# Optimization experiments

Hardware: AMD Instinct MI355X
Metric: run time of the kernel (lower is better)

The kernel has to match this reference:

```python
import jax, jax.numpy as jnp
import numpy as np

# Model dims (match init_kwargs): dim=768, num_heads=12, num_kv_heads=2 -> G=6, head_dim=64
DIM, HKV, G, D = 768, 2, 6, 64


def setup_inputs() -> dict:
    key = jax.random.key(0)
    ks = jax.random.split(key, 9)
    w = 0.02  # init scale for weights
    return {
        "x": jax.random.normal(ks[0], (8, 1024, DIM), dtype=jnp.float32),
        "depth_k": jax.random.normal(ks[1], (8, 1024, HKV, D), dtype=jnp.float32),
        "depth_v": jax.random.normal(ks[2], (8, 1024, HKV, D), dtype=jnp.float32),
        "Wq": jax.random.normal(ks[3], (DIM, DIM), dtype=jnp.float32) * w,
        "bq": jnp.zeros((DIM,), dtype=jnp.float32),
        "Wkv": jax.random.normal(ks[4], (2 * HKV * D, DIM), dtype=jnp.float32) * w,
        "bkv": jnp.zeros((2 * HKV * D,), dtype=jnp.float32),
        "Wproj": jax.random.normal(ks[5], (DIM, DIM), dtype=jnp.float32) * w,
        "bproj": jnp.zeros((DIM,), dtype=jnp.float32),
    }


def reference(x, depth_k, depth_v, Wq, bq, Wkv, bkv, Wproj, bproj):
    B, N, C = x.shape
    scale = D ** -0.5
    # Q projection, GQA groups unfolded into the sequence dim: [B, N*G, Hkv, D]
    q = (x @ Wq.T + bq).reshape(B, N * G, HKV, D)
    # KV projection: [B, N, 2, Hkv, D]
    kv = (x @ Wkv.T + bkv).reshape(B, N, 2, HKV, D)
    k, v = kv[:, :, 0], kv[:, :, 1]
    # Concatenate depth (previous-layer) KV cache along the sequence dim
    k_full = jnp.concatenate([depth_k, k], axis=1)  # [B, N_cache+N, Hkv, D]
    v_full = jnp.concatenate([depth_v, v], axis=1)
    # Full (non-causal) attention per kv head over the unfolded query sequence
    scores = jnp.einsum('bqhd,bkhd->bhqk', q, k_full) * scale  # [B, Hkv, N*G, Kv]
    attn = jax.nn.softmax(scores, axis=-1)
    o = jnp.einsum('bhqk,bkhd->bqhd', attn, v_full)  # [B, N*G, Hkv, D]
    out = o.reshape(B, N, C) @ Wproj.T + bproj  # fold G*Hkv*D back to C=dim
    return out, k, v
```

## Files before the change

kernel.cpp:

```cpp
#include <hip/hip_runtime.h>

using sh8 = __attribute__((ext_vector_type(8))) short;
using sh4 = __attribute__((ext_vector_type(4))) short;
using fx4 = __attribute__((ext_vector_type(4))) float;

#define MFMA(a,b,c)   __builtin_amdgcn_mfma_f32_16x16x32_bf16((a),(b),(c),0,0,0)
#define MFMA16(a,b,c) __builtin_amdgcn_mfma_f32_16x16x16bf16_1k((a),(b),(c),0,0,0)

__device__ __forceinline__ short f2bf(float f) {
    union { float f; unsigned u; } v; v.f = f;
    return (short)((v.u + 0x7fffu + ((v.u >> 16) & 1u)) >> 16);
}

__device__ __forceinline__ unsigned bfpair(float lo, float hi) {
    unsigned ul = __float_as_uint(lo) + 0x8000u;
    unsigned uh = __float_as_uint(hi) + 0x8000u;
    return __builtin_amdgcn_perm(uh, ul, 0x07060302);
}

__device__ __forceinline__ sh8 pack8(float4 a, float4 b) {
    union { unsigned u[4]; sh8 s; } r;
    r.u[0] = bfpair(a.x, a.y);
    r.u[1] = bfpair(a.z, a.w);
    r.u[2] = bfpair(b.x, b.y);
    r.u[3] = bfpair(b.z, b.w);
    return r.s;
}

__device__ __forceinline__ sh4 lo4(sh8 v) { return __builtin_shufflevector(v, v, 0, 1, 2, 3); }
__device__ __forceinline__ sh4 hi4(sh8 v) { return __builtin_shufflevector(v, v, 4, 5, 6, 7); }

#define QSCALE 0.18033688011112042f


__global__ __launch_bounds__(256) void qgemm_k(const float* __restrict__ x,
                                               const float* __restrict__ Wq,
                                               const float* __restrict__ bq,
                                               short* __restrict__ q_ws)
{
    __shared__ alignas(16) short Al[128 * 40];
    __shared__ alignas(16) short Bl[128 * 40];
    const int t    = threadIdx.x;
    const int wave = t >> 6, lane = t & 63;
    const int wm   = wave >> 1, wn = wave & 1;
    const int lhi  = lane >> 4, llo = lane & 15;
    const int bm   = blockIdx.y * 128, bn = blockIdx.x * 128;

    const int srow = t >> 1, scol = (t & 1) * 16;
    const float* ap = x  + (size_t)(bm + srow) * 768 + scol;
    const float* bp = Wq + (size_t)(bn + srow) * 768 + scol;

    fx4 zero = {0.f, 0.f, 0.f, 0.f};
    fx4 acc[4][4];
    #pragma unroll
    for (int i = 0; i < 4; ++i)
        #pragma unroll
        for (int j = 0; j < 4; ++j) acc[i][j] = zero;

    float4 pa0 = *(const float4*)(ap);     float4 pa1 = *(const float4*)(ap + 4);
    float4 pa2 = *(const float4*)(ap + 8); float4 pa3 = *(const float4*)(ap + 12);
    float4 pb0 = *(const float4*)(bp);     float4 pb1 = *(const float4*)(bp + 4);
    float4 pb2 = *(const float4*)(bp + 8); float4 pb3 = *(const float4*)(bp + 12);

    for (int k0 = 0; k0 < 768; k0 += 32) {
        __syncthreads();
        *(sh8*)&Al[srow*40 + scol]     = pack8(pa0, pa1);
        *(sh8*)&Al[srow*40 + scol + 8] = pack8(pa2, pa3);
        *(sh8*)&Bl[srow*40 + scol]     = pack8(pb0, pb1);
        *(sh8*)&Bl[srow*40 + scol + 8] = pack8(pb2, pb3);
        __syncthreads();
        if (k0 + 32 < 768) {
            pa0 = *(const float4*)(ap + k0+32);     pa1 = *(const float4*)(ap + k0+36);
            pa2 = *(const float4*)(ap + k0+40);     pa3 = *(const float4*)(ap + k0+44);
            pb0 = *(const float4*)(bp + k0+32);     pb1 = *(const float4*)(bp + k0+36);
            pb2 = *(const float4*)(bp + k0+40);     pb3 = *(const float4*)(bp + k0+44);
        }
        sh8 af[4], bf[4];
        #pragma unroll
        for (int mt = 0; mt < 4; ++mt)
            af[mt] = *(const sh8*)&Al[(wm*64 + mt*16 + llo)*40 + lhi*8];
        #pragma unroll
        for (int nt = 0; nt < 4; ++nt)
            bf[nt] = *(const sh8*)&Bl[(wn*64 + nt*16 + llo)*40 + lhi*8];
        #pragma unroll
        for (int mt = 0; mt < 4; ++mt)
            #pragma unroll
            for (int nt = 0; nt < 4; ++nt)
                acc[mt][nt] = MFMA(af[mt], bf[nt], acc[mt][nt]);
    }

    #pragma unroll
    for (int nt = 0; nt < 4; ++nt) {
        const int c = bn + wn*64 + nt*16 + llo;
        const float bias = bq[c];
        const int g = c >> 7, h = (c >> 6) & 1, d = c & 63;
        #pragma unroll
        for (int mt = 0; mt < 4; ++mt) {
            const int m0 = bm + wm*64 + mt*16 + lhi*4;
            #pragma unroll
            for (int r = 0; r < 4; ++r) {
                const int m = m0 + r;
                const int b = m >> 10, n = m & 1023;
                const float val = (acc[mt][nt][r] + bias) * QSCALE;
                q_ws[((size_t)(b*2 + h)*6144 + n*6 + g)*64 + d] = f2bf(val);
            }
        }
    }
}

__global__ __launch_bounds__(256) void kvgemm_k(const float* __restrict__ x,
                                                const float* __restrict__ Wkv,
                                                const float* __restrict__ bkv,
                                                float* __restrict__ ok,
                                                float* __restrict__ ov,
                                                short* __restrict__ k_ws,
                                                short* __restrict__ vT_ws)
{
    __shared__ alignas(16) short Al[128 * 40];
    __shared__ alignas(16) short Bl[128 * 40];
    const int t    = threadIdx.x;
    const int wave = t >> 6, lane = t & 63;
    const int wm   = wave >> 1, wn = wave & 1;
    const int lhi  = lane >> 4, llo = lane & 15;
    const int bm   = blockIdx.y * 128, bn = blockIdx.x * 128;

    const int srow = t >> 1, scol = (t & 1) * 16;
    const float* ap = x   + (size_t)(bm + srow) * 768 + scol;
    const float* bp = Wkv + (size_t)(bn + srow) * 768 + scol;

    fx4 zero = {0.f, 0.f, 0.f, 0.f};
    fx4 acc[4][4];
    #pragma unroll
    for (int i = 0; i < 4; ++i)
        #pragma unroll
        for (int j = 0; j < 4; ++j) acc[i][j] = zero;

    float4 pa0 = *(const float4*)(ap);     float4 pa1 = *(const float4*)(ap + 4);
    float4 pa2 = *(const float4*)(ap + 8); float4 pa3 = *(const float4*)(ap + 12);
    float4 pb0 = *(const float4*)(bp);     float4 pb1 = *(const float4*)(bp + 4);
    float4 pb2 = *(const float4*)(bp + 8); float4 pb3 = *(const float4*)(bp + 12);

    for (int k0 = 0; k0 < 768; k0 += 32) {
        __syncthreads();
        *(sh8*)&Al[srow*40 + scol]     = pack8(pa0, pa1);
        *(sh8*)&Al[srow*40 + scol + 8] = pack8(pa2, pa3);
        *(sh8*)&Bl[srow*40 + scol]     = pack8(pb0, pb1);
        *(sh8*)&Bl[srow*40 + scol + 8] = pack8(pb2, pb3);
        __syncthreads();
        if (k0 + 32 < 768) {
            pa0 = *(const float4*)(ap + k0+32);     pa1 = *(const float4*)(ap + k0+36);
            pa2 = *(const float4*)(ap + k0+40);     pa3 = *(const float4*)(ap + k0+44);
            pb0 = *(const float4*)(bp + k0+32);     pb1 = *(const float4*)(bp + k0+36);
            pb2 = *(const float4*)(bp + k0+40);     pb3 = *(const float4*)(bp + k0+44);
        }
        sh8 af[4], bf[4];
        #pragma unroll
        for (int mt = 0; mt < 4; ++mt)
            af[mt] = *(const sh8*)&Al[(wm*64 + mt*16 + llo)*40 + lhi*8];
        #pragma unroll
        for (int nt = 0; nt < 4; ++nt)
            bf[nt] = *(const sh8*)&Bl[(wn*64 + nt*16 + llo)*40 + lhi*8];
        #pragma unroll
        for (int mt = 0; mt < 4; ++mt)
            #pragma unroll
            for (int nt = 0; nt < 4; ++nt)
                acc[mt][nt] = MFMA(af[mt], bf[nt], acc[mt][nt]);
    }

    #pragma unroll
    for (int nt = 0; nt < 4; ++nt) {
        const int c = bn + wn*64 + nt*16 + llo;
        const float bias = bkv[c];
        const int s = c >> 7, h = (c >> 6) & 1, d = c & 63;
        #pragma unroll
        for (int mt = 0; mt < 4; ++mt) {
            const int m0 = bm + wm*64 + mt*16 + lhi*4;
            const int b = m0 >> 10, n0 = m0 & 1023;
            float vals[4];
            #pragma unroll
            for (int r = 0; r < 4; ++r) vals[r] = acc[mt][nt][r] + bias;
            if (s == 0) {
                #pragma unroll
                for (int r = 0; r < 4; ++r) {
                    ok[((size_t)(b*1024 + n0 + r)*2 + h)*64 + d] = vals[r];
                    k_ws[((size_t)(b*2 + h)*2048 + 1024 + n0 + r)*64 + d] = f2bf(vals[r]);
                }
            } else {
                #pragma unroll
                for (int r = 0; r < 4; ++r)
                    ov[((size_t)(b*1024 + n0 + r)*2 + h)*64 + d] = vals[r];
                short4 pk = make_short4(f2bf(vals[0]), f2bf(vals[1]),
                                        f2bf(vals[2]), f2bf(vals[3]));
                *(short4*)&vT_ws[((size_t)((b*2 + h)*64 + d))*2048 + 1024 + n0] = pk;
            }
        }
    }
}

__global__ __launch_bounds__(256) void castdepth_k(const float* __restrict__ dk,
                                                   const float* __restrict__ dv,
                                                   short* __restrict__ k_ws,
                                                   short* __restrict__ vT_ws)
{
    const int t = threadIdx.x;
    if (blockIdx.x < 1024) {
        const size_t idx4 = ((size_t)blockIdx.x * 256 + t) * 4;
        const int b  = (int)(idx4 >> 17);
        const int rm = (int)(idx4 & 131071);
        const int tt = rm >> 7, h = (rm >> 6) & 1, d = rm & 63;
        float4 v = *(const float4*)(dk + idx4);
        short4 pk = make_short4(f2bf(v.x), f2bf(v.y), f2bf(v.z), f2bf(v.w));
        *(short4*)&k_ws[((size_t)(b*2 + h)*2048 + tt)*64 + d] = pk;
    } else {
        __shared__ alignas(16) short tl[64][72];
        const int tile = blockIdx.x - 1024;
        const int bh = tile >> 4, tb = tile & 15;
        const int b = bh >> 1, h = bh & 1, t0 = tb * 64;
        const int tt = t >> 2, d0 = (t & 3) * 16;
        const float* src = dv + ((size_t)(b*1024 + t0 + tt)*2 + h)*64 + d0;
        float4 v0 = *(const float4*)(src);
        float4 v1 = *(const float4*)(src + 4);
        float4 v2 = *(const float4*)(src + 8);
        float4 v3 = *(const float4*)(src + 12);
        *(sh8*)&tl[tt][d0]     = pack8(v0, v1);
        *(sh8*)&tl[tt][d0 + 8] = pack8(v2, v3);
        __syncthreads();
        const int d = t >> 2, ts0 = (t & 3) * 16;
        sh8 o0, o1;
        #pragma unroll
        for (int i = 0; i < 8; ++i) o0[i] = tl[ts0 + i][d];
        #pragma unroll
        for (int i = 0; i < 8; ++i) o1[i] = tl[ts0 + 8 + i][d];
        short* dst = vT_ws + ((size_t)((b*2 + h)*64 + d))*2048 + t0 + ts0;
        *(sh8*)dst       = o0;
        *(sh8*)(dst + 8) = o1;
    }
}

__global__ __launch_bounds__(256) void attn_k(const short* __restrict__ q_ws,
                                              const short* __restrict__ k_ws,
                                              const short* __restrict__ vT_ws,
                                              short* __restrict__ o_ws)
{
    __shared__ alignas(16) short Kl[64][72];
    __shared__ alignas(16) short Vt[64][72];
    const int t    = threadIdx.x;
    const int wave = t >> 6, lane = t & 63;
    const int lhi  = lane >> 4, llo = lane & 15;
    const int bh   = blockIdx.y;
    const int b    = bh >> 1, h = bh & 1;
    const int qt   = blockIdx.x;

    const short* qb = q_ws + ((size_t)bh*6144 + qt*128 + wave*32) * 64;
    sh8 qf[2][2];
    #pragma unroll
    for (int s = 0; s < 2; ++s) {
        qf[s][0] = *(const sh8*)(qb + (s*16 + llo)*64 + lhi*8);
        qf[s][1] = *(const sh8*)(qb + (s*16 + llo)*64 + lhi*8 + 32);
    }

    const short* kbase = k_ws  + (size_t)bh * 2048 * 64;
    const short* vbase = vT_ws + (size_t)bh * 64 * 2048;

    const int urow = t >> 3, uc = t & 7;
    const int vc1  = ((uc & 1) * 2) * 16 + (uc >> 1) * 4;

    const short* kp = kbase + t * 8;
    const short* vp = vbase + (size_t)urow * 2048 + uc * 8;

    sh8 kpre0 = *(const sh8*)(kp);
    sh8 kpre1 = *(const sh8*)(kp + 2048);
    sh8 vpre0 = *(const sh8*)(vp);
    sh8 vpre1 = *(const sh8*)(vp + 65536);

    fx4 zero = {0.f, 0.f, 0.f, 0.f};
    fx4 oacc[2][4];
    #pragma unroll
    for (int s = 0; s < 2; ++s)
        #pragma unroll
        for (int dt = 0; dt < 4; ++dt) oacc[s][dt] = zero;
    float lsum[2] = {0.f, 0.f};

    for (int kb = 0; kb < 32; ++kb) {
        __syncthreads();
        *(sh8*)&Kl[urow][uc*8]         = kpre0;
        *(sh8*)&Kl[urow + 32][uc*8]    = kpre1;
        *(sh4*)&Vt[urow][vc1]          = lo4(vpre0);
        *(sh4*)&Vt[urow][vc1 + 16]     = hi4(vpre0);
        *(sh4*)&Vt[urow + 32][vc1]     = lo4(vpre1);
        *(sh4*)&Vt[urow + 32][vc1 + 16]= hi4(vpre1);
        __syncthreads();

        if (kb < 31) {
            kpre0 = *(const sh8*)(kp + (kb+1)*4096);
            kpre1 = *(const sh8*)(kp + (kb+1)*4096 + 2048);
            vpre0 = *(const sh8*)(vp + (kb+1)*64);
            vpre1 = *(const sh8*)(vp + (kb+1)*64 + 65536);
        }

        sh4 vts[4][4];
        #pragma unroll
        for (int dt = 0; dt < 4; ++dt) {
            sh8 va = *(const sh8*)&Vt[dt*16 + llo][lhi*16];
            sh8 vb = *(const sh8*)&Vt[dt*16 + llo][lhi*16 + 8];
            vts[0][dt] = lo4(va); vts[1][dt] = hi4(va);
            vts[2][dt] = lo4(vb); vts[3][dt] = hi4(vb);
        }

        #pragma unroll
        for (int nt = 0; nt < 4; ++nt) {
            sh8 kf0 = *(const sh8*)&Kl[nt*16 + llo][lhi*8];
            sh8 kf1 = *(const sh8*)&Kl[nt*16 + llo][lhi*8 + 32];
            #pragma unroll
            for (int s = 0; s < 2; ++s) {
                fx4 st = MFMA(kf0, qf[s][0], zero);
                st     = MFMA(kf1, qf[s][1], st);
                float p0 = __builtin_amdgcn_exp2f(st[0]);
                float p1 = __builtin_amdgcn_exp2f(st[1]);
                float p2 = __builtin_amdgcn_exp2f(st[2]);
                float p3 = __builtin_amdgcn_exp2f(st[3]);
                lsum[s] += (p0 + p1) + (p2 + p3);
                union { unsigned u[2]; sh4 s4; } pu;
                pu.u[0] = bfpair(p0, p1);
                pu.u[1] = bfpair(p2, p3);
                #pragma unroll
                for (int dt = 0; dt < 4; ++dt)
                    oacc[s][dt] = MFMA16(pu.s4, vts[nt][dt], oacc[s][dt]);
            }
        }
    }

    float inv[2];
    #pragma unroll
    for (int s = 0; s < 2; ++s) {
        float v = lsum[s];
        v += __shfl_xor(v, 16, 64);
        v += __shfl_xor(v, 32, 64);
        inv[s] = 1.0f / v;
    }

    #pragma unroll
    for (int s = 0; s < 2; ++s) {
        #pragma unroll
        for (int r = 0; r < 4; ++r) {
            const float iq = __shfl(inv[s], lhi*4 + r, 64);
            const int qi = qt*128 + wave*32 + s*16 + lhi*4 + r;
            const int n = qi / 6, g = qi % 6;
            short* orow = o_ws + ((size_t)(b*1024 + n))*768 + g*128 + h*64;
            #pragma unroll
            for (int dt = 0; dt < 4; ++dt)
                orow[dt*16 + llo] = f2bf(oacc[s][dt][r] * iq);
        }
    }
}

__global__ __launch_bounds__(256) void projgemm_k(const short* __restrict__ o_ws,
                                                  const float* __restrict__ Wp,
                                                  const float* __restrict__ bpj,
                                                  float* __restrict__ out)
{
    __shared__ alignas(16) short Al[128 * 40];
    __shared__ alignas(16) short Bl[128 * 40];
    const int t    = threadIdx.x;
    const int wave = t >> 6, lane = t & 63;
    const int wm   = wave >> 1, wn = wave & 1;
    const int lhi  = lane >> 4, llo = lane & 15;
    const int bm   = blockIdx.y * 128, bn = blockIdx.x * 128;

    const int srow = t >> 1, scol = (t & 1) * 16;
    const short* ap = o_ws + (size_t)(bm + srow) * 768 + scol;
    const float* bp = Wp   + (size_t)(bn + srow) * 768 + scol;

    fx4 zero = {0.f, 0.f, 0.f, 0.f};
    fx4 acc[4][4];
    #pragma unroll
    for (int i = 0; i < 4; ++i)
        #pragma unroll
        for (int j = 0; j < 4; ++j) acc[i][j] = zero;

    sh8 qa0 = *(const sh8*)(ap), qa1 = *(const sh8*)(ap + 8);
    float4 pb0 = *(const float4*)(bp);     float4 pb1 = *(const float4*)(bp + 4);
    float4 pb2 = *(const float4*)(bp + 8); float4 pb3 = *(const float4*)(bp + 12);

    for (int k0 = 0; k0 < 768; k0 += 32) {
        __syncthreads();
        *(sh8*)&Al[srow*40 + scol]     = qa0;
        *(sh8*)&Al[srow*40 + scol + 8] = qa1;
        *(sh8*)&Bl[srow*40 + scol]     = pack8(pb0, pb1);
        *(sh8*)&Bl[srow*40 + scol + 8] = pack8(pb2, pb3);
        __syncthreads();
        if (k0 + 32 < 768) {
            qa0 = *(const sh8*)(ap + k0+32);  qa1 = *(const sh8*)(ap + k0+40);
            pb0 = *(const float4*)(bp + k0+32);  pb1 = *(const float4*)(bp + k0+36);
            pb2 = *(const float4*)(bp + k0+40);  pb3 = *(const float4*)(bp + k0+44);
        }
        sh8 af[4], bf[4];
        #pragma unroll
        for (int mt = 0; mt < 4; ++mt)
            af[mt] = *(const sh8*)&Al[(wm*64 + mt*16 + llo)*40 + lhi*8];
        #pragma unroll
        for (int nt = 0; nt < 4; ++nt)
            bf[nt] = *(const sh8*)&Bl[(wn*64 + nt*16 + llo)*40 + lhi*8];
        #pragma unroll
        for (int mt = 0; mt < 4; ++mt)
            #pragma unroll
            for (int nt = 0; nt < 4; ++nt)
                acc[mt][nt] = MFMA(af[mt], bf[nt], acc[mt][nt]);
    }

    #pragma unroll
    for (int nt = 0; nt < 4; ++nt) {
        const int c = bn + wn*64 + nt*16 + llo;
        const float bias = bpj[c];
        #pragma unroll
        for (int mt = 0; mt < 4; ++mt) {
            const int m0 = bm + wm*64 + mt*16 + lhi*4;
            #pragma unroll
            for (int r = 0; r < 4; ++r)
                out[(size_t)(m0 + r)*768 + c] = acc[mt][nt][r] + bias;
        }
    }
}

extern "C" void kernel_launch(void* const* d_in, const int* in_sizes, int n_in,
                              void* d_out, int out_size, void* d_ws, size_t ws_size,
                              hipStream_t stream)
{
    const float* x   = (const float*)d_in[0];
    const float* dk  = (const float*)d_in[1];
    const float* dv  = (const float*)d_in[2];
    const float* Wq  = (const float*)d_in[3];
    const float* bq  = (const float*)d_in[4];
    const float* Wkv = (const float*)d_in[5];
    const float* bkv = (const float*)d_in[6];
    const float* Wp  = (const float*)d_in[7];
    const float* bpj = (const float*)d_in[8];

    float* out = (float*)d_out;
    float* ok  = out + 6291456;
    float* ov  = out + 7340032;

    char* ws = (char*)d_ws;
    short* q_ws  = (short*)(ws);
    short* k_ws  = (short*)(ws + 12582912);
    short* vT_ws = (short*)(ws + 16777216);
    short* o_ws  = (short*)(ws + 20971520);

    qgemm_k    <<<dim3(6, 64), 256, 0, stream>>>(x, Wq, bq, q_ws);
    kvgemm_k   <<<dim3(2, 64), 256, 0, stream>>>(x, Wkv, bkv, ok, ov, k_ws, vT_ws);
    castdepth_k<<<dim3(1280),  256, 0, stream>>>(dk, dv, k_ws, vT_ws);
    attn_k     <<<dim3(48, 16), 256, 0, stream>>>(q_ws, k_ws, vT_ws, o_ws);
    projgemm_k <<<dim3(6, 64), 256, 0, stream>>>(o_ws, Wp, bpj, out);
}
```

Baseline: 254.3 us.

## Merge Q/KV GEMMs and depth cast into one kernel; double-buffer attention LDS

The Q projection, KV projection and depth-cache cast kernels are combined into a single launch that dispatches on block index. This removes two launches and lets the independent pieces run on the GPU at the same time. Separately, the attention kernel now double-buffers its K/V tiles in LDS. Each next tile is written after the compute, so there is one barrier per iteration instead of two. This doubles attention LDS use, which may lower occupancy.

Measured after the change: 229.2 us. -9.8%, faster.

```diff
diff --git a/kernel.cpp b/kernel.cpp
--- a/kernel.cpp
+++ b/kernel.cpp
@@ -32,179 +32,128 @@
 
 #define QSCALE 0.18033688011112042f
 
-
-__global__ __launch_bounds__(256) void qgemm_k(const float* __restrict__ x,
-                                               const float* __restrict__ Wq,
-                                               const float* __restrict__ bq,
-                                               short* __restrict__ q_ws)
+__global__ __launch_bounds__(256) void prep_k(const float* __restrict__ x,
+                                              const float* __restrict__ Wq,
+                                              const float* __restrict__ bq,
+                                              const float* __restrict__ Wkv,
+                                              const float* __restrict__ bkv,
+                                              const float* __restrict__ dk,
+                                              const float* __restrict__ dv,
+                                              float* __restrict__ ok,
+                                              float* __restrict__ ov,
+                                              short* __restrict__ q_ws,
+                                              short* __restrict__ k_ws,
+                                              short* __restrict__ vT_ws)
 {
     __shared__ alignas(16) short Al[128 * 40];
     __shared__ alignas(16) short Bl[128 * 40];
-    const int t    = threadIdx.x;
-    const int wave = t >> 6, lane = t & 63;
-    const int wm   = wave >> 1, wn = wave & 1;
-    const int lhi  = lane >> 4, llo = lane & 15;
-    const int bm   = blockIdx.y * 128, bn = blockIdx.x * 128;
-
-    const int srow = t >> 1, scol = (t & 1) * 16;
-    const float* ap = x  + (size_t)(bm + srow) * 768 + scol;
-    const float* bp = Wq + (size_t)(bn + srow) * 768 + scol;
-
-    fx4 zero = {0.f, 0.f, 0.f, 0.f};
-    fx4 acc[4][4];
-    #pragma unroll
-    for (int i = 0; i < 4; ++i)
-        #pragma unroll
-        for (int j = 0; j < 4; ++j) acc[i][j] = zero;
-
-    float4 pa0 = *(const float4*)(ap);     float4 pa1 = *(const float4*)(ap + 4);
-    float4 pa2 = *(const float4*)(ap + 8); float4 pa3 = *(const float4*)(ap + 12);
-    float4 pb0 = *(const float4*)(bp);     float4 pb1 = *(const float4*)(bp + 4);
-    float4 pb2 = *(const float4*)(bp + 8); float4 pb3 = *(const float4*)(bp + 12);
-
-    for (int k0 = 0; k0 < 768; k0 += 32) {
-        __syncthreads();
-        *(sh8*)&Al[srow*40 + scol]     = pack8(pa0, pa1);
-        *(sh8*)&Al[srow*40 + scol + 8] = pack8(pa2, pa3);
-        *(sh8*)&Bl[srow*40 + scol]     = pack8(pb0, pb1);
-        *(sh8*)&Bl[srow*40 + scol + 8] = pack8(pb2, pb3);
-        __syncthreads();
-        if (k0 + 32 < 768) {
-            pa0 = *(const float4*)(ap + k0+32);     pa1 = *(const float4*)(ap + k0+36);
-            pa2 = *(const float4*)(ap + k0+40);     pa3 = *(const float4*)(ap + k0+44);
-            pb0 = *(const float4*)(bp + k0+32);     pb1 = *(const float4*)(bp + k0+36);
-            pb2 = *(const float4*)(bp + k0+40);     pb3 = *(const float4*)(bp + k0+44);
-        }
-        sh8 af[4], bf[4];
-        #pragma unroll
-        for (int mt = 0; mt < 4; ++mt)
-            af[mt] = *(const sh8*)&Al[(wm*64 + mt*16 + llo)*40 + lhi*8];
-        #pragma unroll
-        for (int nt = 0; nt < 4; ++nt)
-            bf[nt] = *(const sh8*)&Bl[(wn*64 + nt*16 + llo)*40 + lhi*8];
-        #pragma unroll
-        for (int mt = 0; mt < 4; ++mt)
+    const int blk = blockIdx.x;
+    const int t   = threadIdx.x;
+
+    if (blk < 512) {
+        const bool isq = (blk < 384);
+        const int  i   = isq ? blk : blk - 384;
+        const int  nbx = isq ? 6 : 2;
+        const int  bm  = (i / nbx) * 128, bn = (i % nbx) * 128;
+        const float* Wmat = isq ? Wq : Wkv;
+
+        const int wave = t >> 6, lane = t & 63;
+        const int wm   = wave >> 1, wn = wave & 1;
+        const int lhi  = lane >> 4, llo = lane & 15;
+
+        const int srow = t >> 1, scol = (t & 1) * 16;
+        const float* ap = x    + (size_t)(bm + srow) * 768 + scol;
+        const float* bp = Wmat + (size_t)(bn + srow) * 768 + scol;
+
+        fx4 zero = {0.f, 0.f, 0.f, 0.f};
+        fx4 acc[4][4];
+        #pragma unroll
+        for (int a = 0; a < 4; ++a)
+            #pragma unroll
+            for (int b2 = 0; b2 < 4; ++b2) acc[a][b2] = zero;
+
+        float4 pa0 = *(const float4*)(ap);     float4 pa1 = *(const float4*)(ap + 4);
+        float4 pa2 = *(const float4*)(ap + 8); float4 pa3 = *(const float4*)(ap + 12);
+        float4 pb0 = *(const float4*)(bp);     float4 pb1 = *(const float4*)(bp + 4);
+        float4 pb2 = *(const float4*)(bp + 8); float4 pb3 = *(const float4*)(bp + 12);
+
+        for (int k0 = 0; k0 < 768; k0 += 32) {
+            __syncthreads();
+            *(sh8*)&Al[srow*40 + scol]     = pack8(pa0, pa1);
+            *(sh8*)&Al[srow*40 + scol + 8] = pack8(pa2, pa3);
+            *(sh8*)&Bl[srow*40 + scol]     = pack8(pb0, pb1);
+            *(sh8*)&Bl[srow*40 + scol + 8] = pack8(pb2, pb3);
+            __syncthreads();
+            if (k0 + 32 < 768) {
+                pa0 = *(const float4*)(ap + k0+32);  pa1 = *(const float4*)(ap + k0+36);
+                pa2 = *(const float4*)(ap + k0+40);  pa3 = *(const float4*)(ap + k0+44);
+                pb0 = *(const float4*)(bp + k0+32);  pb1 = *(const float4*)(bp + k0+36);
+                pb2 = *(const float4*)(bp + k0+40);  pb3 = *(const float4*)(bp + k0+44);
+            }
+            sh8 af[4], bf[4];
+            #pragma unroll
+            for (int mt = 0; mt < 4; ++mt)
+                af[mt] = *(const sh8*)&Al[(wm*64 + mt*16 + llo)*40 + lhi*8];
             #pragma unroll
             for (int nt = 0; nt < 4; ++nt)
-                acc[mt][nt] = MFMA(af[mt], bf[nt], acc[mt][nt]);
-    }
-
-    #pragma unroll
-    for (int nt = 0; nt < 4; ++nt) {
-        const int c = bn + wn*64 + nt*16 + llo;
-        const float bias = bq[c];
-        const int g = c >> 7, h = (c >> 6) & 1, d = c & 63;
-        #pragma unroll
-        for (int mt = 0; mt < 4; ++mt) {
-            const int m0 = bm + wm*64 + mt*16 + lhi*4;
-            #pragma unroll
-            for (int r = 0; r < 4; ++r) {
-                const int m = m0 + r;
-                const int b = m >> 10, n = m & 1023;
-                const float val = (acc[mt][nt][r] + bias) * QSCALE;
-                q_ws[((size_t)(b*2 + h)*6144 + n*6 + g)*64 + d] = f2bf(val);
+                bf[nt] = *(const sh8*)&Bl[(wn*64 + nt*16 + llo)*40 + lhi*8];
+            #pragma unroll
+            for (int mt = 0; mt < 4; ++mt)
+                #pragma unroll
+                for (int nt = 0; nt < 4; ++nt)
+                    acc[mt][nt] = MFMA(af[mt], bf[nt], acc[mt][nt]);
+        }
+
+        if (isq) {
+            #pragma unroll
+            for (int nt = 0; nt < 4; ++nt) {
+                const int c = bn + wn*64 + nt*16 + llo;
+                const float bias = bq[c];
+                const int g = c >> 7, h = (c >> 6) & 1, d = c & 63;
+                #pragma unroll
+                for (int mt = 0; mt < 4; ++mt) {
+                    const int m0 = bm + wm*64 + mt*16 + lhi*4;
+                    #pragma unroll
+                    for (int r = 0; r < 4; ++r) {
+                        const int m = m0 + r;
+                        const int b = m >> 10, n = m & 1023;
+                        const float val = (acc[mt][nt][r] + bias) * QSCALE;
+                        q_ws[((size_t)(b*2 + h)*6144 + n*6 + g)*64 + d] = f2bf(val);
+                    }
+                }
             }
-        }
-    }
-}
-
-__global__ __launch_bounds__(256) void kvgemm_k(const float* __restrict__ x,
-                                                const float* __restrict__ Wkv,
-                                                const float* __restrict__ bkv,
-                                                float* __restrict__ ok,
-                                                float* __restrict__ ov,
-                                                short* __restrict__ k_ws,
-                                                short* __restrict__ vT_ws)
-{
-    __shared__ alignas(16) short Al[128 * 40];
-    __shared__ alignas(16) short Bl[128 * 40];
-    const int t    = threadIdx.x;
-    const int wave = t >> 6, lane = t & 63;
-    const int wm   = wave >> 1, wn = wave & 1;
-    const int lhi  = lane >> 4, llo = lane & 15;
-    const int bm   = blockIdx.y * 128, bn = blockIdx.x * 128;
-
-    const int srow = t >> 1, scol = (t & 1) * 16;
-    const float* ap = x   + (size_t)(bm + srow) * 768 + scol;
-    const float* bp = Wkv + (size_t)(bn + srow) * 768 + scol;
-
-    fx4 zero = {0.f, 0.f, 0.f, 0.f};
-    fx4 acc[4][4];
-    #pragma unroll
-    for (int i = 0; i < 4; ++i)
-        #pragma unroll
-        for (int j = 0; j < 4; ++j) acc[i][j] = zero;
-
-    float4 pa0 = *(const float4*)(ap);     float4 pa1 = *(const float4*)(ap + 4);
-    float4 pa2 = *(const float4*)(ap + 8); float4 pa3 = *(const float4*)(ap + 12);
-    float4 pb0 = *(const float4*)(bp);     float4 pb1 = *(const float4*)(bp + 4);
-    float4 pb2 = *(const float4*)(bp + 8); float4 pb3 = *(const float4*)(bp + 12);
-
-    for (int k0 = 0; k0 < 768; k0 += 32) {
-        __syncthreads();
-        *(sh8*)&Al[srow*40 + scol]     = pack8(pa0, pa1);
-        *(sh8*)&Al[srow*40 + scol + 8] = pack8(pa2, pa3);
-        *(sh8*)&Bl[srow*40 + scol]     = pack8(pb0, pb1);
-        *(sh8*)&Bl[srow*40 + scol + 8] = pack8(pb2, pb3);
-        __syncthreads();
-        if (k0 + 32 < 768) {
-            pa0 = *(const float4*)(ap + k0+32);     pa1 = *(const float4*)(ap + k0+36);
-            pa2 = *(const float4*)(ap + k0+40);     pa3 = *(const float4*)(ap + k0+44);
-            pb0 = *(const float4*)(bp + k0+32);     pb1 = *(const float4*)(bp + k0+36);
-            pb2 = *(const float4*)(bp + k0+40);     pb3 = *(const float4*)(bp + k0+44);
-        }
-        sh8 af[4], bf[4];
-        #pragma unroll
-        for (int mt = 0; mt < 4; ++mt)
-            af[mt] = *(const sh8*)&Al[(wm*64 + mt*16 + llo)*40 + lhi*8];
-        #pragma unroll
-        for (int nt = 0; nt < 4; ++nt)
-            bf[nt] = *(const sh8*)&Bl[(wn*64 + nt*16 + llo)*40 + lhi*8];
-        #pragma unroll
-        for (int mt = 0; mt < 4; ++mt)
-            #pragma unroll
-            for (int nt = 0; nt < 4; ++nt)
-                acc[mt][nt] = MFMA(af[mt], bf[nt], acc[mt][nt]);
-    }
-
-    #pragma unroll
-    for (int nt = 0; nt < 4; ++nt) {
-        const int c = bn + wn*64 + nt*16 + llo;
-        const float bias = bkv[c];
-        const int s = c >> 7, h = (c >> 6) & 1, d = c & 63;
-        #pragma unroll
-        for (int mt = 0; mt < 4; ++mt) {
-            const int m0 = bm + wm*64 + mt*16 + lhi*4;
-            const int b = m0 >> 10, n0 = m0 & 1023;
-            float vals[4];
-            #pragma unroll
-            for (int r = 0; r < 4; ++r) vals[r] = acc[mt][nt][r] + bias;
-            if (s == 0) {
+        } else {
+            #pragma unroll
+            for (int nt = 0; nt < 4; ++nt) {
+                const int c = bn + wn*64 + nt*16 + llo;
+                const float bias = bkv[c];
+                const int s = c >> 7, h = (c >> 6) & 1, d = c & 63;
                 #pragma unroll
-                for (int r = 0; r < 4; ++r) {
-                    ok[((size_t)(b*1024 + n0 + r)*2 + h)*64 + d] = vals[r];
-                    k_ws[((size_t)(b*2 + h)*2048 + 1024 + n0 + r)*64 + d] = f2bf(vals[r]);
+                for (int mt = 0; mt < 4; ++mt) {
+                    const int m0 = bm + wm*64 + mt*16 + lhi*4;
+                    const int b = m0 >> 10, n0 = m0 & 1023;
+                    float vals[4];
+                    #pragma unroll
+                    for (int r = 0; r < 4; ++r) vals[r] = acc[mt][nt][r] + bias;
+                    if (s == 0) {
+                        #pragma unroll
+                        for (int r = 0; r < 4; ++r) {
+                            ok[((size_t)(b*1024 + n0 + r)*2 + h)*64 + d] = vals[r];
+                            k_ws[((size_t)(b*2 + h)*2048 + 1024 + n0 + r)*64 + d] = f2bf(vals[r]);
+                        }
+                    } else {
+                        #pragma unroll
+                        for (int r = 0; r < 4; ++r)
+                            ov[((size_t)(b*1024 + n0 + r)*2 + h)*64 + d] = vals[r];
+                        short4 pk = make_short4(f2bf(vals[0]), f2bf(vals[1]),
+                                                f2bf(vals[2]), f2bf(vals[3]));
+                        *(short4*)&vT_ws[((size_t)((b*2 + h)*64 + d))*2048 + 1024 + n0] = pk;
+                    }
                 }
-            } else {
-                #pragma unroll
-                for (int r = 0; r < 4; ++r)
-                    ov[((size_t)(b*1024 + n0 + r)*2 + h)*64 + d] = vals[r];
-                short4 pk = make_short4(f2bf(vals[0]), f2bf(vals[1]),
-                                        f2bf(vals[2]), f2bf(vals[3]));
-                *(short4*)&vT_ws[((size_t)((b*2 + h)*64 + d))*2048 + 1024 + n0] = pk;
             }
         }
-    }
-}
-
-__global__ __launch_bounds__(256) void castdepth_k(const float* __restrict__ dk,
-                                                   const float* __restrict__ dv,
-                                                   short* __restrict__ k_ws,
-                                                   short* __restrict__ vT_ws)
-{
-    const int t = threadIdx.x;
-    if (blockIdx.x < 1024) {
-        const size_t idx4 = ((size_t)blockIdx.x * 256 + t) * 4;
+    } else if (blk < 1536) {
+        const size_t idx4 = ((size_t)(blk - 512) * 256 + t) * 4;
         const int b  = (int)(idx4 >> 17);
         const int rm = (int)(idx4 & 131071);
         const int tt = rm >> 7, h = (rm >> 6) & 1, d = rm & 63;
@@ -212,8 +161,8 @@
         short4 pk = make_short4(f2bf(v.x), f2bf(v.y), f2bf(v.z), f2bf(v.w));
         *(short4*)&k_ws[((size_t)(b*2 + h)*2048 + tt)*64 + d] = pk;
     } else {
-        __shared__ alignas(16) short tl[64][72];
-        const int tile = blockIdx.x - 1024;
+        short (*tl)[72] = (short (*)[72])Al;
+        const int tile = blk - 1536;
         const int bh = tile >> 4, tb = tile & 15;
         const int b = bh >> 1, h = bh & 1, t0 = tb * 64;
         const int tt = t >> 2, d0 = (t & 3) * 16;
@@ -242,8 +191,8 @@
                                               const short* __restrict__ vT_ws,
                                               short* __restrict__ o_ws)
 {
-    __shared__ alignas(16) short Kl[64][72];
-    __shared__ alignas(16) short Vt[64][72];
+    __shared__ alignas(16) short Kl[2][64][72];
+    __shared__ alignas(16) short Vt[2][64][72];
     const int t    = threadIdx.x;
     const int wave = t >> 6, lane = t & 63;
     const int lhi  = lane >> 4, llo = lane & 15;
@@ -268,10 +217,19 @@
     const short* kp = kbase + t * 8;
     const short* vp = vbase + (size_t)urow * 2048 + uc * 8;
 
-    sh8 kpre0 = *(const sh8*)(kp);
-    sh8 kpre1 = *(const sh8*)(kp + 2048);
-    sh8 vpre0 = *(const sh8*)(vp);
-    sh8 vpre1 = *(const sh8*)(vp + 65536);
+    {
+        sh8 k0 = *(const sh8*)(kp);
+        sh8 k1 = *(const sh8*)(kp + 2048);
+        sh8 v0 = *(const sh8*)(vp);
+        sh8 v1 = *(const sh8*)(vp + 65536);
+        *(sh8*)&Kl[0][urow][uc*8]          = k0;
+        *(sh8*)&Kl[0][urow + 32][uc*8]     = k1;
+        *(sh4*)&Vt[0][urow][vc1]           = lo4(v0);
+        *(sh4*)&Vt[0][urow][vc1 + 16]      = hi4(v0);
+        *(sh4*)&Vt[0][urow + 32][vc1]      = lo4(v1);
+        *(sh4*)&Vt[0][urow + 32][vc1 + 16] = hi4(v1);
+    }
+    __syncthreads();
 
     fx4 zero = {0.f, 0.f, 0.f, 0.f};
     fx4 oacc[2][4];
@@ -282,35 +240,29 @@
     float lsum[2] = {0.f, 0.f};
 
     for (int kb = 0; kb < 32; ++kb) {
-        __syncthreads();
-        *(sh8*)&Kl[urow][uc*8]         = kpre0;
-        *(sh8*)&Kl[urow + 32][uc*8]    = kpre1;
-        *(sh4*)&Vt[urow][vc1]          = lo4(vpre0);
-        *(sh4*)&Vt[urow][vc1 + 16]     = hi4(vpre0);
-        *(sh4*)&Vt[urow + 32][vc1]     = lo4(vpre1);
-        *(sh4*)&Vt[urow + 32][vc1 + 16]= hi4(vpre1);
-        __syncthreads();
-
+        const int cur = kb & 1, nxt = cur ^ 1;
+
+        sh8 kn0, kn1, vn0, vn1;
         if (kb < 31) {
-            kpre0 = *(const sh8*)(kp + (kb+1)*4096);
-            kpre1 = *(const sh8*)(kp + (kb+1)*4096 + 2048);
-            vpre0 = *(const sh8*)(vp + (kb+1)*64);
-            vpre1 = *(const sh8*)(vp + (kb+1)*64 + 65536);
+            kn0 = *(const sh8*)(kp + (kb+1)*4096);
+            kn1 = *(const sh8*)(kp + (kb+1)*4096 + 2048);
+            vn0 = *(const sh8*)(vp + (kb+1)*64);
+            vn1 = *(const sh8*)(vp + (kb+1)*64 + 65536);
         }
 
         sh4 vts[4][4];
         #pragma unroll
         for (int dt = 0; dt < 4; ++dt) {
-            sh8 va = *(const sh8*)&Vt[dt*16 + llo][lhi*16];
-            sh8 vb = *(const sh8*)&Vt[dt*16 + llo][lhi*16 + 8];
+            sh8 va = *(const sh8*)&Vt[cur][dt*16 + llo][lhi*16];
+            sh8 vb = *(const sh8*)&Vt[cur][dt*16 + llo][lhi*16 + 8];
             vts[0][dt] = lo4(va); vts[1][dt] = hi4(va);
             vts[2][dt] = lo4(vb); vts[3][dt] = hi4(vb);
         }
 
         #pragma unroll
         for (int nt = 0; nt < 4; ++nt) {
-            sh8 kf0 = *(const sh8*)&Kl[nt*16 + llo][lhi*8];
-            sh8 kf1 = *(const sh8*)&Kl[nt*16 + llo][lhi*8 + 32];
+            sh8 kf0 = *(const sh8*)&Kl[cur][nt*16 + llo][lhi*8];
+            sh8 kf1 = *(const sh8*)&Kl[cur][nt*16 + llo][lhi*8 + 32];
             #pragma unroll
             for (int s = 0; s < 2; ++s) {
                 fx4 st = MFMA(kf0, qf[s][0], zero);
@@ -328,6 +280,16 @@
                     oacc[s][dt] = MFMA16(pu.s4, vts[nt][dt], oacc[s][dt]);
             }
         }
+
+        if (kb < 31) {
+            *(sh8*)&Kl[nxt][urow][uc*8]          = kn0;
+            *(sh8*)&Kl[nxt][urow + 32][uc*8]     = kn1;
+            *(sh4*)&Vt[nxt][urow][vc1]           = lo4(vn0);
+            *(sh4*)&Vt[nxt][urow][vc1 + 16]      = hi4(vn0);
+            *(sh4*)&Vt[nxt][urow + 32][vc1]      = lo4(vn1);
+            *(sh4*)&Vt[nxt][urow + 32][vc1 + 16] = hi4(vn1);
+        }
+        __syncthreads();
     }
 
     float inv[2];
@@ -446,9 +408,8 @@
     short* vT_ws = (short*)(ws + 16777216);
     short* o_ws  = (short*)(ws + 20971520);
 
-    qgemm_k    <<<dim3(6, 64), 256, 0, stream>>>(x, Wq, bq, q_ws);
-    kvgemm_k   <<<dim3(2, 64), 256, 0, stream>>>(x, Wkv, bkv, ok, ov, k_ws, vT_ws);
-    castdepth_k<<<dim3(1280),  256, 0, stream>>>(dk, dv, k_ws, vT_ws);
+    prep_k     <<<dim3(1792),   256, 0, stream>>>(x, Wq, bq, Wkv, bkv, dk, dv,
+                                                  ok, ov, q_ws, k_ws, vT_ws);
     attn_k     <<<dim3(48, 16), 256, 0, stream>>>(q_ws, k_ws, vT_ws, o_ws);
-    projgemm_k <<<dim3(6, 64), 256, 0, stream>>>(o_ws, Wp, bpj, out);
-}
+    projgemm_k <<<dim3(6, 64),  256, 0, stream>>>(o_ws, Wp, bpj, out);
+}
```
